# Kernel optimization log

Measured on AMD Instinct MI355X. Metric: run time of the kernel, lower is better.

Reference implementation:

```python
import jax, jax.numpy as jnp
import numpy as np

INPUT_DIM, HIDDEN, HEADS = 310, 64, 8
WINDOW, PERIOD = 5, 3
NEG_INF = -jnp.inf


def _masks(seq_len):
    i = jnp.arange(seq_len)[:, None]
    j = jnp.arange(seq_len)[None, :]
    local = jnp.abs(i - j) <= WINDOW
    sparse = (j % PERIOD == 0) | (i == j)
    to_add = lambda m: jnp.where(m, 0.0, NEG_INF).astype(jnp.float32)
    return to_add(local), to_add(sparse)


def _mha(xp, in_w, in_b, out_w, out_b, mask):
    # xp: [B,S,E]; in_w: [3E,E]; out_w: [E,E]; mask: [S,S] additive
    B, S, E = xp.shape
    d = E // HEADS
    qkv = xp @ in_w.T + in_b                      # [B,S,3E]
    q, k, v = jnp.split(qkv, 3, axis=-1)
    split_heads = lambda t: t.reshape(B, S, HEADS, d).transpose(0, 2, 1, 3)
    q, k, v = split_heads(q), split_heads(k), split_heads(v)
    scores = jnp.einsum('bhqd,bhkd->bhqk', q, k) / jnp.sqrt(jnp.float32(d))
    scores = scores + mask                         # broadcast [S,S]
    attn = jax.nn.softmax(scores, axis=-1)
    o = jnp.einsum('bhqk,bhkd->bhqd', attn, v)
    o = o.transpose(0, 2, 1, 3).reshape(B, S, E)
    return o @ out_w.T + out_b


def setup_inputs() -> dict:
    key = jax.random.key(0)
    ks = jax.random.split(key, 16)
    E = HIDDEN
    s = lambda fan: 1.0 / np.sqrt(fan)
    u = lambda k, shape, fan: jax.random.uniform(k, shape, jnp.float32, -s(fan), s(fan))
    return {
        'x': jax.random.normal(ks[0], (16, 1024, INPUT_DIM), jnp.float32),
        'proj_w': u(ks[1], (E, INPUT_DIM), INPUT_DIM),
        'proj_b': u(ks[2], (E,), INPUT_DIM),
        'loc_in_w': u(ks[3], (3 * E, E), E),
        'loc_in_b': jnp.zeros((3 * E,), jnp.float32),
        'loc_out_w': u(ks[4], (E, E), E),
        'loc_out_b': jnp.zeros((E,), jnp.float32),
        'glob_in_w': u(ks[5], (3 * E, E), E),
        'glob_in_b': jnp.zeros((3 * E,), jnp.float32),
        'glob_out_w': u(ks[6], (E, E), E),
        'glob_out_b': jnp.zeros((E,), jnp.float32),
        'fusion_w': u(ks[7], (E, 2 * E), 2 * E),
        'fusion_b': u(ks[8], (E,), 2 * E),
        'pool_w1': u(ks[9], (E // 2, E), E),
        'pool_b1': u(ks[10], (E // 2,), E),
        'pool_w2': u(ks[11], (1, E // 2), E // 2),
        'pool_b2': u(ks[12], (1,), E // 2),
    }


def reference(x, proj_w, proj_b, loc_in_w, loc_in_b, loc_out_w, loc_out_b,
              glob_in_w, glob_in_b, glob_out_w, glob_out_b,
              fusion_w, fusion_b, pool_w1, pool_b1, pool_w2, pool_b2):
    B, S, _ = x.shape
    local_mask, sparse_mask = _masks(S)
    xp = x @ proj_w.T + proj_b                     # [B,S,E]
    local_out = _mha(xp, loc_in_w, loc_in_b, loc_out_w, loc_out_b, local_mask)
    global_out = _mha(xp, glob_in_w, glob_in_b, glob_out_w, glob_out_b, sparse_mask)
    fused = jnp.concatenate([local_out, global_out], axis=-1) @ fusion_w.T + fusion_b
    scores = jnp.tanh(fused @ pool_w1.T + pool_b1) @ pool_w2.T + pool_b2  # [B,S,1]
    w = jax.nn.softmax(scores, axis=1)             # softmax over seq dim
    return jnp.sum(fused * w, axis=1)              # [B,E]
```

## Files before the change

### kernel.cpp

```cpp
#include <hip/hip_runtime.h>
#include <hip/hip_bf16.h>


typedef __attribute__((ext_vector_type(8))) short short8;
typedef __attribute__((ext_vector_type(4))) float float4v;

#define INV_SQRT8 0.3535533905932738f

__device__ __forceinline__ float4 ld4(const float* p) { return *(const float4*)p; }

__device__ __forceinline__ float4 f4fma(float s, float4 w, float4 a) {
  a.x = fmaf(s, w.x, a.x); a.y = fmaf(s, w.y, a.y);
  a.z = fmaf(s, w.z, a.z); a.w = fmaf(s, w.w, a.w);
  return a;
}

__device__ __forceinline__ short f2bf(float x) {
  __hip_bfloat16 b = __float2bfloat16(x);
  unsigned short u; __builtin_memcpy(&u, &b, 2);
  return (short)u;
}
__device__ __forceinline__ float bf2f(short s) {
  return __uint_as_float(((unsigned)(unsigned short)s) << 16);
}
__device__ __forceinline__ void bsplit(float x, short& h, short& l) {
  h = f2bf(x);
  l = f2bf(x - bf2f(h));
}

__global__ __launch_bounds__(256) void prep_w(
    const float* __restrict__ pw, const float* __restrict__ liw,
    const float* __restrict__ giw, const float* __restrict__ fw,
    const float* __restrict__ low, const float* __restrict__ gow,
    const float* __restrict__ lob, const float* __restrict__ gob,
    const float* __restrict__ fb,
    short* __restrict__ wb, float* __restrict__ bc, float* __restrict__ numden,
    short* __restrict__ VTh, short* __restrict__ VTl)
{
  unsigned idx = blockIdx.x * 256 + threadIdx.x;
  if (idx < 53248u) {
    float v; unsigned ho, lo_;
    if (idx < 20480u) {
      unsigned r = idx / 320u, k = idx - r * 320u;
      v = (k < 310u) ? pw[r * 310u + k] : 0.f;
      ho = 0u + idx; lo_ = 20480u + idx;
    } else if (idx < 32768u) {
      unsigned i = idx - 20480u; v = liw[i]; ho = 40960u + i; lo_ = 53248u + i;
    } else if (idx < 45056u) {
      unsigned i = idx - 32768u; v = giw[i]; ho = 65536u + i; lo_ = 77824u + i;
    } else {
      unsigned i = idx - 45056u;
      unsigned n = i >> 7, k = i & 127u;
      float s = 0.f;
      if (k < 64u) {
        for (int e = 0; e < 64; e++) s += fw[n * 128 + e] * low[e * 64 + k];
      } else {
        for (int e = 0; e < 64; e++) s += fw[n * 128 + 64 + e] * gow[e * 64 + (k - 64u)];
      }
      v = s; ho = 90112u + i; lo_ = 98304u + i;
    }
    short h, l; bsplit(v, h, l);
    wb[ho] = h; wb[lo_] = l;
    if (idx < 64u) {
      float b = fb[idx];
      for (int e = 0; e < 64; e++)
        b += lob[e] * fw[idx * 128 + e] + gob[e] * fw[idx * 128 + 64 + e];
      bc[idx] = b;
    }
    if (idx < 1041u) numden[idx] = 0.f;
  } else {
    unsigned t = idx - 53248u;
    if (t < 370688u) {
      unsigned pos; short hv = 0;
      if (t < 360448u) {
        unsigned bh = t / 2816u;
        unsigned rem = t - bh * 2816u;
        unsigned n8 = rem / 352u;
        unsigned kk = rem - n8 * 352u;
        pos = (bh * 16u + 8u + n8) * 352u + kk;
        if (n8 == 0u) hv = (short)0x3F80;
      } else {
        unsigned t2 = t - 360448u;
        unsigned bh = t2 / 80u;
        unsigned rem = t2 - bh * 80u;
        unsigned n = rem / 10u;
        unsigned kk = 342u + (rem - n * 10u);
        pos = (bh * 16u + n) * 352u + kk;
      }
      VTh[pos] = hv; VTl[pos] = 0;
    }
  }
}

__global__ __launch_bounds__(256) void gemm_proj_qkv(
    const float* __restrict__ X,
    const short* __restrict__ PWh, const short* __restrict__ PWl,
    const float* __restrict__ pb,
    const short* __restrict__ LWh, const short* __restrict__ LWl,
    const short* __restrict__ GWh, const short* __restrict__ GWl,
    const float* __restrict__ lb, const float* __restrict__ gb,
    float* __restrict__ qkv_l, float* __restrict__ qkv_g,
    short* __restrict__ KH, short* __restrict__ KL,
    short* __restrict__ VTh, short* __restrict__ VTl)
{
  __shared__ __align__(16) short XPH[16][72];
  __shared__ __align__(16) short XPL[16][72];
  const int lane = threadIdx.x & 63;
  const int w = threadIdx.x >> 6;
  const int q = lane >> 4, r = lane & 15;
  const int m0 = blockIdx.x * 16;

  float4v accp;
  {
    float bv = pb[w * 16 + r];
    float4v t = {bv, bv, bv, bv};
    accp = t;
  }
  const float* arow = X + (size_t)(m0 + r) * 310;
  #pragma unroll
  for (int ks = 0; ks < 10; ks++) {
    const int k0 = ks * 32 + q * 8;
    float av[8];
    if (ks < 9) {
      const float* ap = arow + k0;
      #pragma unroll
      for (int t = 0; t < 4; t++) {
        float2 f = *(const float2*)(ap + t * 2);
        av[t*2] = f.x; av[t*2+1] = f.y;
      }
    } else {
      #pragma unroll
      for (int j = 0; j < 8; j++) {
        int kidx = k0 + j;
        av[j] = (kidx < 310) ? arow[kidx] : 0.f;
      }
    }
    short8 ah, al;
    #pragma unroll
    for (int i = 0; i < 8; i++) { short h, l; bsplit(av[i], h, l); ah[i]=h; al[i]=l; }
    short8 bh = *(const short8*)(PWh + (size_t)(w * 16 + r) * 320 + k0);
    short8 bl = *(const short8*)(PWl + (size_t)(w * 16 + r) * 320 + k0);
    accp = __builtin_amdgcn_mfma_f32_16x16x32_bf16(al, bh, accp, 0, 0, 0);
    accp = __builtin_amdgcn_mfma_f32_16x16x32_bf16(ah, bl, accp, 0, 0, 0);
    accp = __builtin_amdgcn_mfma_f32_16x16x32_bf16(ah, bh, accp, 0, 0, 0);
  }
  #pragma unroll
  for (int e = 0; e < 4; e++) {
    short h, l; bsplit(accp[e], h, l);
    XPH[q * 4 + e][w * 16 + r] = h;
    XPL[q * 4 + e][w * 16 + r] = l;
  }
  __syncthreads();

  const int br = w >> 1, hf = w & 1;
  const short* Wh = br ? GWh : LWh;
  const short* Wl = br ? GWl : LWl;
  const float* bb = br ? gb : lb;
  float* qkv = br ? qkv_g : qkv_l;

  float4v acc[6];
  #pragma unroll
  for (int j = 0; j < 6; j++) {
    float bv = bb[(hf * 6 + j) * 16 + r];
    float4v t = {bv, bv, bv, bv};
    acc[j] = t;
  }
  #pragma unroll
  for (int ks = 0; ks < 2; ks++) {
    const int k0 = ks * 32 + q * 8;
    short8 ah = *(const short8*)&XPH[r][k0];
    short8 al = *(const short8*)&XPL[r][k0];
    #pragma unroll
    for (int j = 0; j < 6; j++) {
      const int nf = hf * 6 + j;
      short8 bh = *(const short8*)(Wh + (size_t)(nf * 16 + r) * 64 + k0);
      short8 bl = *(const short8*)(Wl + (size_t)(nf * 16 + r) * 64 + k0);
      acc[j] = __builtin_amdgcn_mfma_f32_16x16x32_bf16(al, bh, acc[j], 0, 0, 0);
      acc[j] = __builtin_amdgcn_mfma_f32_16x16x32_bf16(ah, bl, acc[j], 0, 0, 0);
      acc[j] = __builtin_amdgcn_mfma_f32_16x16x32_bf16(ah, bh, acc[j], 0, 0, 0);
    }
  }

  const int b = m0 >> 10;
  const int bh8 = b * 8;
  #pragma unroll
  for (int e = 0; e < 4; e++) {
    const int row = m0 + q * 4 + e;
    const int i = row & 1023;
    #pragma unroll
    for (int j = 0; j < 6; j++) {
      const int nf = hf * 6 + j;
      qkv[(size_t)row * 192 + nf * 16 + r] = acc[j][e];
    }
    if (br == 1 && i % 3 == 0) {
      const int kk = i / 3;
      #pragma unroll
      for (int j = 0; j < 6; j++) {
        const int nf = hf * 6 + j;
        if (nf >= 4) {
          const int col = nf * 16 + r;
          float v = acc[j][e];
          short h, l; bsplit(v, h, l);
          if (col < 128) {
            const int ck = col - 64;
            const int hh = ck >> 3, d = ck & 7;
            KH[(size_t)(bh8 + hh) * 2816 + kk * 8 + d] = h;
            KL[(size_t)(bh8 + hh) * 2816 + kk * 8 + d] = l;
          } else {
            const int cv = col - 128;
            const int hh = cv >> 3, d = cv & 7;
            VTh[((size_t)(bh8 + hh) * 16 + d) * 352 + kk] = h;
            VTl[((size_t)(bh8 + hh) * 16 + d) * 352 + kk] = l;
          }
        }
      }
    }
  }
}

__global__ __launch_bounds__(256) void attn(
    const float* __restrict__ qkv_g, const float* __restrict__ qkv_l,
    const short* __restrict__ KH, const short* __restrict__ KL,
    const short* __restrict__ VTh, const short* __restrict__ VTl,
    float* __restrict__ o_g, float* __restrict__ pl, float* __restrict__ o_l)
{
  __shared__ short Pbuf[4][2][2][16][32];
  const int u = blockIdx.x;
  if (u < 2048) {
    const int qt = u & 15, h = (u >> 4) & 7, b = u >> 7;
    const int w = threadIdx.x >> 6, lane = threadIdx.x & 63;
    const int quad = lane >> 4, r = lane & 15;
    const int bh = b * 8 + h;
    const int m0 = qt * 64 + w * 16;

    const short8 z8 = {0,0,0,0,0,0,0,0};
    short8 qh = z8, ql = z8;
    if (quad == 0) {
      const float* qp = qkv_g + (size_t)(b * 1024 + m0 + r) * 192 + h * 8;
      float4 a0 = ld4(qp), a1 = ld4(qp + 4);
      float qv[8] = {a0.x, a0.y, a0.z, a0.w, a1.x, a1.y, a1.z, a1.w};
      #pragma unroll
      for (int d = 0; d < 8; d++) { short hh, ll; bsplit(qv[d], hh, ll); qh[d]=hh; ql[d]=ll; }
    }
    const short* kbase  = KH + (size_t)bh * 2816;
    const short* klbase = KL + (size_t)bh * 2816;
    const short* vhbase = VTh + ((size_t)bh * 16 + r) * 352;
    const short* vlbase = VTl + ((size_t)bh * 16 + r) * 352;

    float4v oacc = {0.f, 0.f, 0.f, 0.f};
    short8 vprev_h = z8, vprev_l = z8;

    for (int kc = 0; kc < 11; kc++) {
      short8 vh = *(const short8*)(vhbase + kc * 32 + quad * 8);
      short8 vl = *(const short8*)(vlbase + kc * 32 + quad * 8);

      short8 pA = z8, pB = z8;
      if (kc > 0) {
        pA = *(const short8*)&Pbuf[w][(kc - 1) & 1][0][r][quad * 8];
        pB = *(const short8*)&Pbuf[w][(kc - 1) & 1][1][r][quad * 8];
      }

      short8 kh0 = z8, kl0 = z8, kh1 = z8, kl1 = z8;
      if (quad == 0) {
        kh0 = *(const short8*)(kbase  + (size_t)(kc * 32 + r) * 8);
        kl0 = *(const short8*)(klbase + (size_t)(kc * 32 + r) * 8);
        kh1 = *(const short8*)(kbase  + (size_t)(kc * 32 + 16 + r) * 8);
        kl1 = *(const short8*)(klbase + (size_t)(kc * 32 + 16 + r) * 8);
      }
      float4v s0 = {0.f,0.f,0.f,0.f}, s1 = {0.f,0.f,0.f,0.f};
      s0 = __builtin_amdgcn_mfma_f32_16x16x32_bf16(qh, kl0, s0, 0, 0, 0);
      s0 = __builtin_amdgcn_mfma_f32_16x16x32_bf16(ql, kh0, s0, 0, 0, 0);
      s0 = __builtin_amdgcn_mfma_f32_16x16x32_bf16(qh, kh0, s0, 0, 0, 0);
      s1 = __builtin_amdgcn_mfma_f32_16x16x32_bf16(qh, kl1, s1, 0, 0, 0);
      s1 = __builtin_amdgcn_mfma_f32_16x16x32_bf16(ql, kh1, s1, 0, 0, 0);
      s1 = __builtin_amdgcn_mfma_f32_16x16x32_bf16(qh, kh1, s1, 0, 0, 0);

      if (kc > 0) {
        oacc = __builtin_amdgcn_mfma_f32_16x16x32_bf16(pA, vprev_l, oacc, 0, 0, 0);
        oacc = __builtin_amdgcn_mfma_f32_16x16x32_bf16(pB, vprev_h, oacc, 0, 0, 0);
        oacc = __builtin_amdgcn_mfma_f32_16x16x32_bf16(pA, vprev_h, oacc, 0, 0, 0);
      }

      const int par = kc & 1;
      const int key0 = kc * 32 + r, key1 = key0 + 16;
      #pragma unroll
      for (int e = 0; e < 4; e++) {
        float p0 = (key0 < 342) ? __expf(s0[e] * INV_SQRT8) : 0.f;
        float p1 = (key1 < 342) ? __expf(s1[e] * INV_SQRT8) : 0.f;
        short h0, l0, h1, l1; bsplit(p0, h0, l0); bsplit(p1, h1, l1);
        const int qloc = quad * 4 + e;
        Pbuf[w][par][0][qloc][r]      = h0;
        Pbuf[w][par][0][qloc][16 + r] = h1;
        Pbuf[w][par][1][qloc][r]      = l0;
        Pbuf[w][par][1][qloc][16 + r] = l1;
      }
      vprev_h = vh; vprev_l = vl;
    }
    {
      short8 pA = *(const short8*)&Pbuf[w][0][0][r][quad * 8];
      short8 pB = *(const short8*)&Pbuf[w][0][1][r][quad * 8];
      oacc = __builtin_amdgcn_mfma_f32_16x16x32_bf16(pA, vprev_l, oacc, 0, 0, 0);
      oacc = __builtin_amdgcn_mfma_f32_16x16x32_bf16(pB, vprev_h, oacc, 0, 0, 0);
      oacc = __builtin_amdgcn_mfma_f32_16x16x32_bf16(pA, vprev_h, oacc, 0, 0, 0);
    }

    #pragma unroll
    for (int e = 0; e < 4; e++) {
      const int orow = b * 1024 + m0 + quad * 4 + e;
      if (r < 8)       o_g[(size_t)orow * 64 + h * 8 + r] = oacc[e];
      else if (r == 8) pl[(size_t)orow * 8 + h] = oacc[e];
    }
  } else {
    int t = (u - 2048) * 256 + threadIdx.x;
    int h = t & 7;
    int i = (t >> 3) & 1023;
    int b = t >> 13;
    const float* base = qkv_l + (size_t)b * 1024 * 192;
    const float* qp = base + (size_t)i * 192 + h * 8;
    float4 q0 = ld4(qp), q1 = ld4(qp + 4);
    float l = 0.f;
    float4 o0 = make_float4(0.f, 0.f, 0.f, 0.f);
    float4 o1 = make_float4(0.f, 0.f, 0.f, 0.f);
    int jlo = i - 5; if (jlo < 0) jlo = 0;
    int jhi = i + 5; if (jhi > 1023) jhi = 1023;
    for (int j = jlo; j <= jhi; j++) {
      const float* kp = base + (size_t)j * 192 + 64 + h * 8;
      float4 k0 = ld4(kp), k1 = ld4(kp + 4);
      float s = q0.x * k0.x + q0.y * k0.y + q0.z * k0.z + q0.w * k0.w
              + q1.x * k1.x + q1.y * k1.y + q1.z * k1.z + q1.w * k1.w;
      float p = __expf(s * INV_SQRT8);
      l += p;
      float4 v0 = ld4(kp + 64), v1 = ld4(kp + 68);
      o0 = f4fma(p, v0, o0);
      o1 = f4fma(p, v1, o1);
    }
    float inv = 1.f / l;
    float* op = o_l + (size_t)(b * 1024 + i) * 64 + h * 8;
    float4 r0, r1;
    r0.x = o0.x * inv; r0.y = o0.y * inv; r0.z = o0.z * inv; r0.w = o0.w * inv;
    r1.x = o1.x * inv; r1.y = o1.y * inv; r1.z = o1.z * inv; r1.w = o1.w * inv;
    *(float4*)op = r0;
    *(float4*)(op + 4) = r1;
  }
}

__global__ __launch_bounds__(256) void gemm_fuse_score(
    const float* __restrict__ o_l, const float* __restrict__ o_g,
    const float* __restrict__ pl, const float* __restrict__ qkv_g,
    const short* __restrict__ Wh, const short* __restrict__ Wl,
    const float* __restrict__ bc,
    const float* __restrict__ pw1, const float* __restrict__ pb1,
    const float* __restrict__ pw2, const float* __restrict__ pb2,
    float* __restrict__ num, float* __restrict__ den,
    unsigned* __restrict__ cnt, float* __restrict__ out)
{
  __shared__ float Ls[32][68];
  __shared__ float partial[4][64];
  __shared__ unsigned lastflag;
  const int tid = threadIdx.x;
  const int lane = tid & 63, w = tid >> 6;
  const int quad = lane >> 4, r = lane & 15;
  const int bx = blockIdx.x;
  const int t = w >> 1, p = w & 1;
  const int m0 = bx * 32 + t * 16;

  float4v acc[2];
  #pragma unroll
  for (int gg = 0; gg < 2; gg++) {
    float bv = bc[(p * 2 + gg) * 16 + r];
    float4v tv = {bv, bv, bv, bv};
    acc[gg] = tv;
  }

  #pragma unroll
  for (int ks = 0; ks < 4; ks++) {
    const int k0 = ks * 32 + quad * 8;
    const int row = m0 + r;
    float av[8];
    if (ks < 2) {
      const float* ap = o_l + (size_t)row * 64 + k0;
      float4 f0 = ld4(ap), f1 = ld4(ap + 4);
      av[0]=f0.x; av[1]=f0.y; av[2]=f0.z; av[3]=f0.w;
      av[4]=f1.x; av[5]=f1.y; av[6]=f1.z; av[7]=f1.w;
    } else {
      const int off = k0 - 64;
      const int h = off >> 3;
      const float* op = o_g + (size_t)row * 64 + off;
      float4 O0 = ld4(op), O1 = ld4(op + 4);
      float l = pl[(size_t)row * 8 + h];
      const int i = row & 1023;
      if (i % 3 != 0) {
        const float* base = qkv_g + (size_t)row * 192;
        const float* qp = base + h * 8;
        const float* kpp = base + 64 + h * 8;
        const float* vp = base + 128 + h * 8;
        float4 q0 = ld4(qp), q1 = ld4(qp + 4);
        float4 k0v = ld4(kpp), k1v = ld4(kpp + 4);
        float s = q0.x*k0v.x + q0.y*k0v.y + q0.z*k0v.z + q0.w*k0v.w
                + q1.x*k1v.x + q1.y*k1v.y + q1.z*k1v.z + q1.w*k1v.w;
        float pd = __expf(s * INV_SQRT8);
        float4 v0 = ld4(vp), v1 = ld4(vp + 4);
        O0 = f4fma(pd, v0, O0); O1 = f4fma(pd, v1, O1);
        l += pd;
      }
      float inv = 1.f / l;
      av[0]=O0.x*inv; av[1]=O0.y*inv; av[2]=O0.z*inv; av[3]=O0.w*inv;
      av[4]=O1.x*inv; av[5]=O1.y*inv; av[6]=O1.z*inv; av[7]=O1.w*inv;
    }
    short8 ah, al;
    #pragma unroll
    for (int i2 = 0; i2 < 8; i2++) { short h2, l2; bsplit(av[i2], h2, l2); ah[i2]=h2; al[i2]=l2; }
    #pragma unroll
    for (int gg = 0; gg < 2; gg++) {
      const int g = p * 2 + gg;
      short8 bh = *(const short8*)(Wh + (size_t)(g * 16 + r) * 128 + k0);
      short8 bl = *(const short8*)(Wl + (size_t)(g * 16 + r) * 128 + k0);
      acc[gg] = __builtin_amdgcn_mfma_f32_16x16x32_bf16(al, bh, acc[gg], 0, 0, 0);
      acc[gg] = __builtin_amdgcn_mfma_f32_16x16x32_bf16(ah, bl, acc[gg], 0, 0, 0);
      acc[gg] = __builtin_amdgcn_mfma_f32_16x16x32_bf16(ah, bh, acc[gg], 0, 0, 0);
    }
  }

  #pragma unroll
  for (int gg = 0; gg < 2; gg++)
    #pragma unroll
    for (int e = 0; e < 4; e++)
      Ls[t * 16 + quad * 4 + e][(p * 2 + gg) * 16 + r] = acc[gg][e];
  __syncthreads();

  const int row31 = lane & 31, half = lane >> 5;
  float4 fr[16];
  #pragma unroll
  for (int e = 0; e < 16; e++) fr[e] = *(float4*)&Ls[row31][e * 4];

  float psc = 0.f;
  #pragma unroll
  for (int jj = 0; jj < 4; jj++) {
    const int j = w * 8 + half * 4 + jj;
    const float* wr = pw1 + j * 64;
    float hj = pb1[j];
    #pragma unroll
    for (int e = 0; e < 16; e++) {
      float4 wv = ld4(wr + e * 4);
      hj += fr[e].x * wv.x + fr[e].y * wv.y + fr[e].z * wv.z + fr[e].w * wv.w;
    }
    float e2 = __expf(2.f * hj);
    psc += ((e2 - 1.f) / (e2 + 1.f)) * pw2[j];
  }
  partial[w][lane] = psc;
  __syncthreads();
  if (w == 0) {
    const int b = bx >> 5;
    float pv = 0.f;
    if (lane < 32) {
      float sc = pb2[0];
      #pragma unroll
      for (int w2 = 0; w2 < 4; w2++)
        sc += partial[w2][lane] + partial[w2][lane + 32];
      pv = __expf(sc);
      #pragma unroll
      for (int e = 0; e < 16; e++) {
        Ls[lane][e*4+0] = pv * fr[e].x; Ls[lane][e*4+1] = pv * fr[e].y;
        Ls[lane][e*4+2] = pv * fr[e].z; Ls[lane][e*4+3] = pv * fr[e].w;
      }
    }
    float colsum = 0.f;
    #pragma unroll 8
    for (int s = 0; s < 32; s++) colsum += Ls[s][lane];
    atomicAdd(&num[b * 64 + lane], colsum);
    float ps = pv;
    #pragma unroll
    for (int off = 32; off > 0; off >>= 1)
      ps += __shfl_xor(ps, off, 64);
    if (lane == 0) atomicAdd(&den[b], ps);
  }

  if (tid == 0) {
    __threadfence();
    lastflag = (atomicAdd(cnt, 1u) == 511u) ? 1u : 0u;
  }
  __syncthreads();
  if (lastflag) {
    __threadfence();
    for (int k = tid; k < 1024; k += 256) {
      float nv = __hip_atomic_load(&num[k], __ATOMIC_RELAXED, __HIP_MEMORY_SCOPE_AGENT);
      float dv = __hip_atomic_load(&den[k >> 6], __ATOMIC_RELAXED, __HIP_MEMORY_SCOPE_AGENT);
      out[k] = nv / dv;
    }
  }
}

extern "C" void kernel_launch(void* const* d_in, const int* in_sizes, int n_in,
                              void* d_out, int out_size, void* d_ws, size_t ws_size,
                              hipStream_t stream)
{
  const float* x          = (const float*)d_in[0];
  const float* proj_w     = (const float*)d_in[1];
  const float* proj_b     = (const float*)d_in[2];
  const float* loc_in_w   = (const float*)d_in[3];
  const float* loc_in_b   = (const float*)d_in[4];
  const float* loc_out_w  = (const float*)d_in[5];
  const float* loc_out_b  = (const float*)d_in[6];
  const float* glob_in_w  = (const float*)d_in[7];
  const float* glob_in_b  = (const float*)d_in[8];
  const float* glob_out_w = (const float*)d_in[9];
  const float* glob_out_b = (const float*)d_in[10];
  const float* fusion_w   = (const float*)d_in[11];
  const float* fusion_b   = (const float*)d_in[12];
  const float* pw1        = (const float*)d_in[13];
  const float* pb1        = (const float*)d_in[14];
  const float* pw2        = (const float*)d_in[15];
  const float* pb2        = (const float*)d_in[16];

  float* ws = (float*)d_ws;
  float* qkv_g = ws;
  float* qkv_l = ws + 4587520;
  float* o_l   = ws + 7733248;
  float* o_g   = ws + 8781824;
  float* pl    = ws + 9830400;
  short* KH    = (short*)(ws + 9961472);
  short* KL    = (short*)(ws + 10141696);
  short* VTh   = (short*)(ws + 10321920);
  short* VTl   = (short*)(ws + 10682368);
  float* bc    = ws + 11042816;
  float* numden= ws + 11042880;
  float* num   = numden;
  float* den   = numden + 1024;
  unsigned* cnt= (unsigned*)(numden + 1040);
  short* wb    = (short*)(ws + 11043921);
  short* projh = wb;           short* projl = wb + 20480;
  short* linh  = wb + 40960;   short* linl  = wb + 53248;
  short* ginh  = wb + 65536;   short* ginl  = wb + 77824;
  short* wfh   = wb + 90112;   short* wfl   = wb + 98304;
  float* out   = (float*)d_out;

  dim3 blk(256);
  prep_w<<<1656, blk, 0, stream>>>(proj_w, loc_in_w, glob_in_w, fusion_w,
                                   loc_out_w, glob_out_w, loc_out_b, glob_out_b,
                                   fusion_b, wb, bc, numden, VTh, VTl);
  gemm_proj_qkv<<<1024, blk, 0, stream>>>(
      x, projh, projl, proj_b, linh, linl, ginh, ginl, loc_in_b, glob_in_b,
      qkv_l, qkv_g, KH, KL, VTh, VTl);
  attn<<<2560, blk, 0, stream>>>(qkv_g, qkv_l, KH, KL, VTh, VTl, o_g, pl, o_l);
  gemm_fuse_score<<<512, blk, 0, stream>>>(
      o_l, o_g, pl, qkv_g, wfh, wfl, bc, pw1, pb1, pw2, pb2, num, den, cnt, out);
}
```

Measured before the change: 183.2 us.

## Fuse four stages into one cooperative persistent kernel with grid syncs

Merges the prep, projection/QKV, attention and fusion/score kernels into a single cooperative launch of 1024 blocks, separated by grid-wide barriers, and falls back to the separate launches if the cooperative launch fails. The aim is to remove the per-kernel launch gaps and tail drain between stages. The cost is the grid-sync overhead, a cap of 4 blocks per CU that may limit registers, and attention work now done in grid-strided loops over 1024 resident blocks instead of 2560 independently scheduled ones.

```diff
diff --git a/kernel.cpp b/kernel.cpp
--- a/kernel.cpp
+++ b/kernel.cpp
@@ -1,5 +1,8 @@
 #include <hip/hip_runtime.h>
 #include <hip/hip_bf16.h>
+#include <hip/hip_cooperative_groups.h>
+
+namespace cg = cooperative_groups;
 
 
 typedef __attribute__((ext_vector_type(8))) short short8;
@@ -28,43 +31,40 @@
   l = f2bf(x - bf2f(h));
 }
 
-__global__ __launch_bounds__(256) void prep_w(
-    const float* __restrict__ pw, const float* __restrict__ liw,
-    const float* __restrict__ giw, const float* __restrict__ fw,
-    const float* __restrict__ low, const float* __restrict__ gow,
-    const float* __restrict__ lob, const float* __restrict__ gob,
-    const float* __restrict__ fb,
-    short* __restrict__ wb, float* __restrict__ bc, float* __restrict__ numden,
-    short* __restrict__ VTh, short* __restrict__ VTl)
-{
-  unsigned idx = blockIdx.x * 256 + threadIdx.x;
+__device__ __forceinline__ void prep_item(
+    unsigned idx,
+    const float* PW, const float* LIW, const float* GIW, const float* FW,
+    const float* LOW, const float* GOW, const float* LOB, const float* GOB,
+    const float* FB,
+    short* wb, float* bc, float* numden, short* VTh, short* VTl)
+{
   if (idx < 53248u) {
     float v; unsigned ho, lo_;
     if (idx < 20480u) {
       unsigned r = idx / 320u, k = idx - r * 320u;
-      v = (k < 310u) ? pw[r * 310u + k] : 0.f;
+      v = (k < 310u) ? PW[r * 310u + k] : 0.f;
       ho = 0u + idx; lo_ = 20480u + idx;
     } else if (idx < 32768u) {
-      unsigned i = idx - 20480u; v = liw[i]; ho = 40960u + i; lo_ = 53248u + i;
+      unsigned i = idx - 20480u; v = LIW[i]; ho = 40960u + i; lo_ = 53248u + i;
     } else if (idx < 45056u) {
-      unsigned i = idx - 32768u; v = giw[i]; ho = 65536u + i; lo_ = 77824u + i;
+      unsigned i = idx - 32768u; v = GIW[i]; ho = 65536u + i; lo_ = 77824u + i;
     } else {
       unsigned i = idx - 45056u;
       unsigned n = i >> 7, k = i & 127u;
       float s = 0.f;
       if (k < 64u) {
-        for (int e = 0; e < 64; e++) s += fw[n * 128 + e] * low[e * 64 + k];
+        for (int e = 0; e < 64; e++) s += FW[n * 128 + e] * LOW[e * 64 + k];
       } else {
-        for (int e = 0; e < 64; e++) s += fw[n * 128 + 64 + e] * gow[e * 64 + (k - 64u)];
+        for (int e = 0; e < 64; e++) s += FW[n * 128 + 64 + e] * GOW[e * 64 + (k - 64u)];
       }
       v = s; ho = 90112u + i; lo_ = 98304u + i;
     }
     short h, l; bsplit(v, h, l);
     wb[ho] = h; wb[lo_] = l;
     if (idx < 64u) {
-      float b = fb[idx];
+      float b = FB[idx];
       for (int e = 0; e < 64; e++)
-        b += lob[e] * fw[idx * 128 + e] + gob[e] * fw[idx * 128 + 64 + e];
+        b += LOB[e] * FW[idx * 128 + e] + GOB[e] * FW[idx * 128 + 64 + e];
       bc[idx] = b;
     }
     if (idx < 1041u) numden[idx] = 0.f;
@@ -92,23 +92,20 @@
   }
 }
 
-__global__ __launch_bounds__(256) void gemm_proj_qkv(
-    const float* __restrict__ X,
-    const short* __restrict__ PWh, const short* __restrict__ PWl,
-    const float* __restrict__ pb,
-    const short* __restrict__ LWh, const short* __restrict__ LWl,
-    const short* __restrict__ GWh, const short* __restrict__ GWl,
-    const float* __restrict__ lb, const float* __restrict__ gb,
-    float* __restrict__ qkv_l, float* __restrict__ qkv_g,
-    short* __restrict__ KH, short* __restrict__ KL,
-    short* __restrict__ VTh, short* __restrict__ VTl)
-{
-  __shared__ __align__(16) short XPH[16][72];
-  __shared__ __align__(16) short XPL[16][72];
-  const int lane = threadIdx.x & 63;
-  const int w = threadIdx.x >> 6;
+__device__ __forceinline__ void proj_qkv_tile(
+    int m0, int tid,
+    short XPH[16][72], short XPL[16][72],
+    const float* X,
+    const short* PWh, const short* PWl, const float* pb,
+    const short* LWh, const short* LWl,
+    const short* GWh, const short* GWl,
+    const float* lb, const float* gb,
+    float* qkv_l, float* qkv_g,
+    short* KH, short* KL, short* VTh, short* VTl)
+{
+  const int lane = tid & 63;
+  const int w = tid >> 6;
   const int q = lane >> 4, r = lane & 15;
-  const int m0 = blockIdx.x * 16;
 
   float4v accp;
   {
@@ -218,17 +215,17 @@
   }
 }
 
-__global__ __launch_bounds__(256) void attn(
-    const float* __restrict__ qkv_g, const float* __restrict__ qkv_l,
-    const short* __restrict__ KH, const short* __restrict__ KL,
-    const short* __restrict__ VTh, const short* __restrict__ VTl,
-    float* __restrict__ o_g, float* __restrict__ pl, float* __restrict__ o_l)
-{
-  __shared__ short Pbuf[4][2][2][16][32];
-  const int u = blockIdx.x;
+__device__ __forceinline__ void attn_unit(
+    int u, int tid,
+    short Pbuf[4][2][2][16][32],
+    const float* qkv_g, const float* qkv_l,
+    const short* KH, const short* KL,
+    const short* VTh, const short* VTl,
+    float* o_g, float* pl, float* o_l)
+{
   if (u < 2048) {
     const int qt = u & 15, h = (u >> 4) & 7, b = u >> 7;
-    const int w = threadIdx.x >> 6, lane = threadIdx.x & 63;
+    const int w = tid >> 6, lane = tid & 63;
     const int quad = lane >> 4, r = lane & 15;
     const int bh = b * 8 + h;
     const int m0 = qt * 64 + w * 16;
@@ -304,14 +301,15 @@
       oacc = __builtin_amdgcn_mfma_f32_16x16x32_bf16(pA, vprev_h, oacc, 0, 0, 0);
     }
 
+    const int quad2 = (tid & 63) >> 4, r2 = tid & 15;
     #pragma unroll
     for (int e = 0; e < 4; e++) {
-      const int orow = b * 1024 + m0 + quad * 4 + e;
-      if (r < 8)       o_g[(size_t)orow * 64 + h * 8 + r] = oacc[e];
-      else if (r == 8) pl[(size_t)orow * 8 + h] = oacc[e];
+      const int orow = b * 1024 + m0 + quad2 * 4 + e;
+      if (r2 < 8)       o_g[(size_t)orow * 64 + h * 8 + r2] = oacc[e];
+      else if (r2 == 8) pl[(size_t)orow * 8 + h] = oacc[e];
     }
   } else {
-    int t = (u - 2048) * 256 + threadIdx.x;
+    int t = (u - 2048) * 256 + tid;
     int h = t & 7;
     int i = (t >> 3) & 1023;
     int b = t >> 13;
@@ -344,23 +342,16 @@
   }
 }
 
-__global__ __launch_bounds__(256) void gemm_fuse_score(
-    const float* __restrict__ o_l, const float* __restrict__ o_g,
-    const float* __restrict__ pl, const float* __restrict__ qkv_g,
-    const short* __restrict__ Wh, const short* __restrict__ Wl,
-    const float* __restrict__ bc,
-    const float* __restrict__ pw1, const float* __restrict__ pb1,
-    const float* __restrict__ pw2, const float* __restrict__ pb2,
-    float* __restrict__ num, float* __restrict__ den,
-    unsigned* __restrict__ cnt, float* __restrict__ out)
-{
-  __shared__ float Ls[32][68];
-  __shared__ float partial[4][64];
-  __shared__ unsigned lastflag;
-  const int tid = threadIdx.x;
+__device__ __forceinline__ void fuse_unit(
+    int bx, int tid,
+    float Ls[32][68], float partial[4][64], unsigned* lastflag,
+    const float* o_l, const float* o_g, const float* pl, const float* qkv_g,
+    const short* Wh, const short* Wl, const float* bc,
+    const float* pw1, const float* pb1, const float* pw2, const float* pb2,
+    float* num, float* den, unsigned* cnt, float* out)
+{
   const int lane = tid & 63, w = tid >> 6;
   const int quad = lane >> 4, r = lane & 15;
-  const int bx = blockIdx.x;
   const int t = w >> 1, p = w & 1;
   const int m0 = bx * 32 + t * 16;
 
@@ -477,10 +468,10 @@
 
   if (tid == 0) {
     __threadfence();
-    lastflag = (atomicAdd(cnt, 1u) == 511u) ? 1u : 0u;
+    *lastflag = (atomicAdd(cnt, 1u) == 511u) ? 1u : 0u;
   }
   __syncthreads();
-  if (lastflag) {
+  if (*lastflag) {
     __threadfence();
     for (int k = tid; k < 1024; k += 256) {
       float nv = __hip_atomic_load(&num[k], __ATOMIC_RELAXED, __HIP_MEMORY_SCOPE_AGENT);
@@ -488,6 +479,121 @@
       out[k] = nv / dv;
     }
   }
+}
+
+__global__ __launch_bounds__(256, 4) void fused_all(
+    const float* __restrict__ X,  const float* __restrict__ PW,
+    const float* __restrict__ PB,
+    const float* __restrict__ LIW, const float* __restrict__ LIB,
+    const float* __restrict__ GIW, const float* __restrict__ GIB,
+    const float* __restrict__ LOW, const float* __restrict__ GOW,
+    const float* __restrict__ LOB, const float* __restrict__ GOB,
+    const float* __restrict__ FW,  const float* __restrict__ FB,
+    const float* __restrict__ PW1, const float* __restrict__ PB1,
+    const float* __restrict__ PW2, const float* __restrict__ PB2,
+    short* __restrict__ wb, float* __restrict__ bc, float* __restrict__ numden,
+    float* __restrict__ qkv_l, float* __restrict__ qkv_g,
+    float* __restrict__ o_l, float* __restrict__ o_g, float* __restrict__ pl,
+    short* __restrict__ KH, short* __restrict__ KL,
+    short* __restrict__ VTh, short* __restrict__ VTl,
+    float* __restrict__ out)
+{
+  __shared__ __align__(16) short XPH[16][72];
+  __shared__ __align__(16) short XPL[16][72];
+  __shared__ short Pbuf[4][2][2][16][32];
+  __shared__ float Ls[32][68];
+  __shared__ float partial[4][64];
+  __shared__ unsigned lastflag;
+
+  cg::grid_group grid = cg::this_grid();
+  const int tid = threadIdx.x;
+  const int bid = blockIdx.x;
+
+  const short* projh = wb;         const short* projl = wb + 20480;
+  const short* linh = wb + 40960;  const short* linl = wb + 53248;
+  const short* ginh = wb + 65536;  const short* ginl = wb + 77824;
+  const short* wfh = wb + 90112;   const short* wfl = wb + 98304;
+  float* num = numden; float* den = numden + 1024;
+  unsigned* cnt = (unsigned*)(numden + 1040);
+
+  for (unsigned idx = (unsigned)bid * 256u + tid; idx < 423936u; idx += 262144u)
+    prep_item(idx, PW, LIW, GIW, FW, LOW, GOW, LOB, GOB, FB,
+              wb, bc, numden, VTh, VTl);
+  grid.sync();
+
+  proj_qkv_tile(bid * 16, tid, XPH, XPL, X, projh, projl, PB,
+                linh, linl, ginh, ginl, LIB, GIB,
+                qkv_l, qkv_g, KH, KL, VTh, VTl);
+  grid.sync();
+
+  for (int u = bid; u < 2560; u += 1024)
+    attn_unit(u, tid, Pbuf, qkv_g, qkv_l, KH, KL, VTh, VTl, o_g, pl, o_l);
+  grid.sync();
+
+  if (bid < 512)
+    fuse_unit(bid, tid, Ls, partial, &lastflag,
+              o_l, o_g, pl, qkv_g, wfh, wfl, bc,
+              PW1, PB1, PW2, PB2, num, den, cnt, out);
+}
+
+__global__ __launch_bounds__(256) void prep_w_k(
+    const float* __restrict__ PW, const float* __restrict__ LIW,
+    const float* __restrict__ GIW, const float* __restrict__ FW,
+    const float* __restrict__ LOW, const float* __restrict__ GOW,
+    const float* __restrict__ LOB, const float* __restrict__ GOB,
+    const float* __restrict__ FB,
+    short* __restrict__ wb, float* __restrict__ bc, float* __restrict__ numden,
+    short* __restrict__ VTh, short* __restrict__ VTl)
+{
+  unsigned idx = blockIdx.x * 256 + threadIdx.x;
+  prep_item(idx, PW, LIW, GIW, FW, LOW, GOW, LOB, GOB, FB,
+            wb, bc, numden, VTh, VTl);
+}
+
+__global__ __launch_bounds__(256) void gemm_proj_qkv_k(
+    const float* __restrict__ X,
+    const short* __restrict__ PWh, const short* __restrict__ PWl,
+    const float* __restrict__ pb,
+    const short* __restrict__ LWh, const short* __restrict__ LWl,
+    const short* __restrict__ GWh, const short* __restrict__ GWl,
+    const float* __restrict__ lb, const float* __restrict__ gb,
+    float* __restrict__ qkv_l, float* __restrict__ qkv_g,
+    short* __restrict__ KH, short* __restrict__ KL,
+    short* __restrict__ VTh, short* __restrict__ VTl)
+{
+  __shared__ __align__(16) short XPH[16][72];
+  __shared__ __align__(16) short XPL[16][72];
+  proj_qkv_tile(blockIdx.x * 16, threadIdx.x, XPH, XPL, X, PWh, PWl, pb,
+                LWh, LWl, GWh, GWl, lb, gb, qkv_l, qkv_g, KH, KL, VTh, VTl);
+}
+
+__global__ __launch_bounds__(256) void attn_k(
+    const float* __restrict__ qkv_g, const float* __restrict__ qkv_l,
+    const short* __restrict__ KH, const short* __restrict__ KL,
+    const short* __restrict__ VTh, const short* __restrict__ VTl,
+    float* __restrict__ o_g, float* __restrict__ pl, float* __restrict__ o_l)
+{
+  __shared__ short Pbuf[4][2][2][16][32];
+  attn_unit(blockIdx.x, threadIdx.x, Pbuf, qkv_g, qkv_l, KH, KL, VTh, VTl,
+            o_g, pl, o_l);
+}
+
+__global__ __launch_bounds__(256) void gemm_fuse_score_k(
+    const float* __restrict__ o_l, const float* __restrict__ o_g,
+    const float* __restrict__ pl, const float* __restrict__ qkv_g,
+    const short* __restrict__ Wh, const short* __restrict__ Wl,
+    const float* __restrict__ bc,
+    const float* __restrict__ pw1, const float* __restrict__ pb1,
+    const float* __restrict__ pw2, const float* __restrict__ pb2,
+    float* __restrict__ num, float* __restrict__ den,
+    unsigned* __restrict__ cnt, float* __restrict__ out)
+{
+  __shared__ float Ls[32][68];
+  __shared__ float partial[4][64];
+  __shared__ unsigned lastflag;
+  fuse_unit(blockIdx.x, threadIdx.x, Ls, partial, &lastflag,
+            o_l, o_g, pl, qkv_g, Wh, Wl, bc, pw1, pb1, pw2, pb2,
+            num, den, cnt, out);
 }
 
 extern "C" void kernel_launch(void* const* d_in, const int* in_sizes, int n_in,
@@ -534,14 +640,33 @@
   short* wfh   = wb + 90112;   short* wfl   = wb + 98304;
   float* out   = (float*)d_out;
 
-  dim3 blk(256);
-  prep_w<<<1656, blk, 0, stream>>>(proj_w, loc_in_w, glob_in_w, fusion_w,
-                                   loc_out_w, glob_out_w, loc_out_b, glob_out_b,
-                                   fusion_b, wb, bc, numden, VTh, VTl);
-  gemm_proj_qkv<<<1024, blk, 0, stream>>>(
-      x, projh, projl, proj_b, linh, linl, ginh, ginl, loc_in_b, glob_in_b,
-      qkv_l, qkv_g, KH, KL, VTh, VTl);
-  attn<<<2560, blk, 0, stream>>>(qkv_g, qkv_l, KH, KL, VTh, VTl, o_g, pl, o_l);
-  gemm_fuse_score<<<512, blk, 0, stream>>>(
-      o_l, o_g, pl, qkv_g, wfh, wfl, bc, pw1, pb1, pw2, pb2, num, den, cnt, out);
-}
+  void* args[] = {
+    (void*)&x, (void*)&proj_w, (void*)&proj_b,
+    (void*)&loc_in_w, (void*)&loc_in_b, (void*)&glob_in_w, (void*)&glob_in_b,
+    (void*)&loc_out_w, (void*)&glob_out_w, (void*)&loc_out_b, (void*)&glob_out_b,
+    (void*)&fusion_w, (void*)&fusion_b,
+    (void*)&pw1, (void*)&pb1, (void*)&pw2, (void*)&pb2,
+    (void*)&wb, (void*)&bc, (void*)&numden,
+    (void*)&qkv_l, (void*)&qkv_g, (void*)&o_l, (void*)&o_g, (void*)&pl,
+    (void*)&KH, (void*)&KL, (void*)&VTh, (void*)&VTl,
+    (void*)&out
+  };
+  hipError_t err = hipLaunchCooperativeKernel(
+      (const void*)fused_all, dim3(1024), dim3(256), args, 0, stream);
+
+  if (err != hipSuccess) {
+    dim3 blk(256);
+    prep_w_k<<<1656, blk, 0, stream>>>(proj_w, loc_in_w, glob_in_w, fusion_w,
+                                       loc_out_w, glob_out_w, loc_out_b,
+                                       glob_out_b, fusion_b, wb, bc, numden,
+                                       VTh, VTl);
+    gemm_proj_qkv_k<<<1024, blk, 0, stream>>>(
+        x, projh, projl, proj_b, linh, linl, ginh, ginl, loc_in_b, glob_in_b,
+        qkv_l, qkv_g, KH, KL, VTh, VTl);
+    attn_k<<<2560, blk, 0, stream>>>(qkv_g, qkv_l, KH, KL, VTh, VTl,
+                                     o_g, pl, o_l);
+    gemm_fuse_score_k<<<512, blk, 0, stream>>>(
+        o_l, o_g, pl, qkv_g, wfh, wfl, bc, pw1, pb1, pw2, pb2,
+        num, den, cnt, out);
+  }
+}
```

Result: slower. 609.0 us (+232.4%).

## Enlarge fusion GEMM tile to 64 rows per block and un-pipeline attention PV

Applied to the files above, without the earlier changes.

The fusion/score kernel now gives each block 64 rows with every wave computing all four output column groups, which halves the block count to 256 and the number of atomic adds into num/den. In exchange each wave does twice the MFMA and pooling work, and the grid shrinks below the CU count. The global attention loop also drops its software-pipelined P·V step: it reloads P from the buffer it just wrote and multiplies it in the same iteration instead of deferring by one chunk, which simplifies the code but exposes LDS latency.

```diff
diff --git a/kernel.cpp b/kernel.cpp
--- a/kernel.cpp
+++ b/kernel.cpp
@@ -248,18 +248,8 @@
     const short* vlbase = VTl + ((size_t)bh * 16 + r) * 352;
 
     float4v oacc = {0.f, 0.f, 0.f, 0.f};
-    short8 vprev_h = z8, vprev_l = z8;
 
     for (int kc = 0; kc < 11; kc++) {
-      short8 vh = *(const short8*)(vhbase + kc * 32 + quad * 8);
-      short8 vl = *(const short8*)(vlbase + kc * 32 + quad * 8);
-
-      short8 pA = z8, pB = z8;
-      if (kc > 0) {
-        pA = *(const short8*)&Pbuf[w][(kc - 1) & 1][0][r][quad * 8];
-        pB = *(const short8*)&Pbuf[w][(kc - 1) & 1][1][r][quad * 8];
-      }
-
       short8 kh0 = z8, kl0 = z8, kh1 = z8, kl1 = z8;
       if (quad == 0) {
         kh0 = *(const short8*)(kbase  + (size_t)(kc * 32 + r) * 8);
@@ -274,12 +264,6 @@
       s1 = __builtin_amdgcn_mfma_f32_16x16x32_bf16(qh, kl1, s1, 0, 0, 0);
       s1 = __builtin_amdgcn_mfma_f32_16x16x32_bf16(ql, kh1, s1, 0, 0, 0);
       s1 = __builtin_amdgcn_mfma_f32_16x16x32_bf16(qh, kh1, s1, 0, 0, 0);
-
-      if (kc > 0) {
-        oacc = __builtin_amdgcn_mfma_f32_16x16x32_bf16(pA, vprev_l, oacc, 0, 0, 0);
-        oacc = __builtin_amdgcn_mfma_f32_16x16x32_bf16(pB, vprev_h, oacc, 0, 0, 0);
-        oacc = __builtin_amdgcn_mfma_f32_16x16x32_bf16(pA, vprev_h, oacc, 0, 0, 0);
-      }
 
       const int par = kc & 1;
       const int key0 = kc * 32 + r, key1 = key0 + 16;
@@ -294,14 +278,13 @@
         Pbuf[w][par][1][qloc][r]      = l0;
         Pbuf[w][par][1][qloc][16 + r] = l1;
       }
-      vprev_h = vh; vprev_l = vl;
-    }
-    {
-      short8 pA = *(const short8*)&Pbuf[w][0][0][r][quad * 8];
-      short8 pB = *(const short8*)&Pbuf[w][0][1][r][quad * 8];
-      oacc = __builtin_amdgcn_mfma_f32_16x16x32_bf16(pA, vprev_l, oacc, 0, 0, 0);
-      oacc = __builtin_amdgcn_mfma_f32_16x16x32_bf16(pB, vprev_h, oacc, 0, 0, 0);
-      oacc = __builtin_amdgcn_mfma_f32_16x16x32_bf16(pA, vprev_h, oacc, 0, 0, 0);
+      short8 pA = *(const short8*)&Pbuf[w][par][0][r][quad * 8];
+      short8 pB = *(const short8*)&Pbuf[w][par][1][r][quad * 8];
+      short8 vh = *(const short8*)(vhbase + kc * 32 + quad * 8);
+      short8 vl = *(const short8*)(vlbase + kc * 32 + quad * 8);
+      oacc = __builtin_amdgcn_mfma_f32_16x16x32_bf16(pA, vl, oacc, 0, 0, 0);
+      oacc = __builtin_amdgcn_mfma_f32_16x16x32_bf16(pB, vh, oacc, 0, 0, 0);
+      oacc = __builtin_amdgcn_mfma_f32_16x16x32_bf16(pA, vh, oacc, 0, 0, 0);
     }
 
     #pragma unroll
@@ -354,22 +337,21 @@
     float* __restrict__ num, float* __restrict__ den,
     unsigned* __restrict__ cnt, float* __restrict__ out)
 {
-  __shared__ float Ls[32][68];
+  __shared__ float Ls[64][68];
   __shared__ float partial[4][64];
   __shared__ unsigned lastflag;
   const int tid = threadIdx.x;
   const int lane = tid & 63, w = tid >> 6;
   const int quad = lane >> 4, r = lane & 15;
   const int bx = blockIdx.x;
-  const int t = w >> 1, p = w & 1;
-  const int m0 = bx * 32 + t * 16;
-
-  float4v acc[2];
-  #pragma unroll
-  for (int gg = 0; gg < 2; gg++) {
-    float bv = bc[(p * 2 + gg) * 16 + r];
-    float4v tv = {bv, bv, bv, bv};
-    acc[gg] = tv;
+  const int m0 = bx * 64 + w * 16;
+
+  float4v acc[4];
+  #pragma unroll
+  for (int g = 0; g < 4; g++) {
+    float bv = bc[g * 16 + r];
+    float4v t = {bv, bv, bv, bv};
+    acc[g] = t;
   }
 
   #pragma unroll
@@ -398,10 +380,10 @@
         float4 k0v = ld4(kpp), k1v = ld4(kpp + 4);
         float s = q0.x*k0v.x + q0.y*k0v.y + q0.z*k0v.z + q0.w*k0v.w
                 + q1.x*k1v.x + q1.y*k1v.y + q1.z*k1v.z + q1.w*k1v.w;
-        float pd = __expf(s * INV_SQRT8);
+        float p = __expf(s * INV_SQRT8);
         float4 v0 = ld4(vp), v1 = ld4(vp + 4);
-        O0 = f4fma(pd, v0, O0); O1 = f4fma(pd, v1, O1);
-        l += pd;
+        O0 = f4fma(p, v0, O0); O1 = f4fma(p, v1, O1);
+        l += p;
       }
       float inv = 1.f / l;
       av[0]=O0.x*inv; av[1]=O0.y*inv; av[2]=O0.z*inv; av[3]=O0.w*inv;
@@ -411,32 +393,30 @@
     #pragma unroll
     for (int i2 = 0; i2 < 8; i2++) { short h2, l2; bsplit(av[i2], h2, l2); ah[i2]=h2; al[i2]=l2; }
     #pragma unroll
-    for (int gg = 0; gg < 2; gg++) {
-      const int g = p * 2 + gg;
+    for (int g = 0; g < 4; g++) {
       short8 bh = *(const short8*)(Wh + (size_t)(g * 16 + r) * 128 + k0);
       short8 bl = *(const short8*)(Wl + (size_t)(g * 16 + r) * 128 + k0);
-      acc[gg] = __builtin_amdgcn_mfma_f32_16x16x32_bf16(al, bh, acc[gg], 0, 0, 0);
-      acc[gg] = __builtin_amdgcn_mfma_f32_16x16x32_bf16(ah, bl, acc[gg], 0, 0, 0);
-      acc[gg] = __builtin_amdgcn_mfma_f32_16x16x32_bf16(ah, bh, acc[gg], 0, 0, 0);
-    }
-  }
-
-  #pragma unroll
-  for (int gg = 0; gg < 2; gg++)
+      acc[g] = __builtin_amdgcn_mfma_f32_16x16x32_bf16(al, bh, acc[g], 0, 0, 0);
+      acc[g] = __builtin_amdgcn_mfma_f32_16x16x32_bf16(ah, bl, acc[g], 0, 0, 0);
+      acc[g] = __builtin_amdgcn_mfma_f32_16x16x32_bf16(ah, bh, acc[g], 0, 0, 0);
+    }
+  }
+
+  #pragma unroll
+  for (int g = 0; g < 4; g++)
     #pragma unroll
     for (int e = 0; e < 4; e++)
-      Ls[t * 16 + quad * 4 + e][(p * 2 + gg) * 16 + r] = acc[gg][e];
+      Ls[w * 16 + quad * 4 + e][g * 16 + r] = acc[g][e];
   __syncthreads();
 
-  const int row31 = lane & 31, half = lane >> 5;
   float4 fr[16];
   #pragma unroll
-  for (int e = 0; e < 16; e++) fr[e] = *(float4*)&Ls[row31][e * 4];
+  for (int e = 0; e < 16; e++) fr[e] = *(float4*)&Ls[lane][e * 4];
 
   float psc = 0.f;
   #pragma unroll
-  for (int jj = 0; jj < 4; jj++) {
-    const int j = w * 8 + half * 4 + jj;
+  for (int jj = 0; jj < 8; jj++) {
+    const int j = w * 8 + jj;
     const float* wr = pw1 + j * 64;
     float hj = pb1[j];
     #pragma unroll
@@ -450,25 +430,20 @@
   partial[w][lane] = psc;
   __syncthreads();
   if (w == 0) {
-    const int b = bx >> 5;
-    float pv = 0.f;
-    if (lane < 32) {
-      float sc = pb2[0];
-      #pragma unroll
-      for (int w2 = 0; w2 < 4; w2++)
-        sc += partial[w2][lane] + partial[w2][lane + 32];
-      pv = __expf(sc);
-      #pragma unroll
-      for (int e = 0; e < 16; e++) {
-        Ls[lane][e*4+0] = pv * fr[e].x; Ls[lane][e*4+1] = pv * fr[e].y;
-        Ls[lane][e*4+2] = pv * fr[e].z; Ls[lane][e*4+3] = pv * fr[e].w;
-      }
+    const int b = bx >> 4;
+    float sc = pb2[0] + partial[0][lane] + partial[1][lane]
+             + partial[2][lane] + partial[3][lane];
+    float p = __expf(sc);
+    #pragma unroll
+    for (int e = 0; e < 16; e++) {
+      Ls[lane][e*4+0] = p * fr[e].x; Ls[lane][e*4+1] = p * fr[e].y;
+      Ls[lane][e*4+2] = p * fr[e].z; Ls[lane][e*4+3] = p * fr[e].w;
     }
     float colsum = 0.f;
     #pragma unroll 8
-    for (int s = 0; s < 32; s++) colsum += Ls[s][lane];
+    for (int s = 0; s < 64; s++) colsum += Ls[s][lane];
     atomicAdd(&num[b * 64 + lane], colsum);
-    float ps = pv;
+    float ps = p;
     #pragma unroll
     for (int off = 32; off > 0; off >>= 1)
       ps += __shfl_xor(ps, off, 64);
@@ -477,7 +452,7 @@
 
   if (tid == 0) {
     __threadfence();
-    lastflag = (atomicAdd(cnt, 1u) == 511u) ? 1u : 0u;
+    lastflag = (atomicAdd(cnt, 1u) == 255u) ? 1u : 0u;
   }
   __syncthreads();
   if (lastflag) {
@@ -542,6 +517,6 @@
       x, projh, projl, proj_b, linh, linl, ginh, ginl, loc_in_b, glob_in_b,
       qkv_l, qkv_g, KH, KL, VTh, VTl);
   attn<<<2560, blk, 0, stream>>>(qkv_g, qkv_l, KH, KL, VTh, VTl, o_g, pl, o_l);
-  gemm_fuse_score<<<512, blk, 0, stream>>>(
+  gemm_fuse_score<<<256, blk, 0, stream>>>(
       o_l, o_g, pl, qkv_g, wfh, wfl, bc, pw1, pb1, pw2, pb2, num, den, cnt, out);
 }
```

Measured after the change: 180.2 us. No clear change (-1.7%).
